# Kernel optimization log

Measured on AMD Instinct MI355X. Metric: run time of the kernel, lower is better.

## Reference

```python
import jax, jax.numpy as jnp
import numpy as np

N, C, H, W = 64, 64, 128, 128
KH, KW = 3, 3


def setup_inputs() -> dict:
    key = jax.random.key(0)
    k1, k2 = jax.random.split(key)
    images = jax.random.normal(k1, (N, C, H, W), dtype=jnp.float32)
    kernels = jax.random.normal(k2, (N, C, KH, KW), dtype=jnp.float32)
    return {"images": images, "kernels": kernels}


def reference(images, kernels):
    # Per-sample conv: image i ([C,H,W]) convolved with kernel i ([C,kh,kw]) -> 1 channel.
    # Equivalent to a grouped conv with N groups:
    #   input  [1, N*C, H, W], weights [N, C, kh, kw], feature_group_count=N
    n, c, h, w = images.shape
    x = images.reshape(1, n * c, h, w)
    out = jax.lax.conv_general_dilated(
        x, kernels,
        window_strides=(1, 1),
        padding='VALID',
        dimension_numbers=('NCHW', 'OIHW', 'NCHW'),
        feature_group_count=n,
    )  # [1, N, H', W']
    return out.reshape(n, 1, out.shape[2], out.shape[3])
```

## Files before the change

kernel.cpp:

```cpp
#include <hip/hip_runtime.h>


#define NS   64
#define CCH  64
#define HH   128
#define WW   128
#define OHH  126
#define OWW  126
#define CHS  (HH * WW)

__global__ __launch_bounds__(256, 2)
void ImageWiseConv2d_direct(const float* __restrict__ img,
                            const float* __restrict__ ker,
                            float* __restrict__ out)
{
    const int tid = threadIdx.x;
    const int bx  = blockIdx.x;
    const int bt  = bx & 7;
    const int n   = bx >> 3;
    const int h0  = bt * 16;

    const int r0 = (tid >> 5) << 1;
    const int c0 = (tid & 31) << 2;

    int ihr = h0 + r0;
    if (ihr > HH - 4) ihr = HH - 4;
    const int bOff = (c0 < 124) ? 4 : 2;

    const float* p0 = img + (((n * CCH) * HH) + ihr) * WW + c0;
    const float* kp = ker + (n * CCH) * 9;

    float a00 = 0.f, a01 = 0.f, a02 = 0.f, a03 = 0.f;
    float a10 = 0.f, a11 = 0.f, a12 = 0.f, a13 = 0.f;

    float4 A0, A1, A2, A3;
    float2 B0, B1, B2, B3;
    A0 = *(const float4*)(p0);
    A1 = *(const float4*)(p0 + WW);
    A2 = *(const float4*)(p0 + 2 * WW);
    A3 = *(const float4*)(p0 + 3 * WW);
    B0 = *(const float2*)(p0 + bOff);
    B1 = *(const float2*)(p0 + WW + bOff);
    B2 = *(const float2*)(p0 + 2 * WW + bOff);
    B3 = *(const float2*)(p0 + 3 * WW + bOff);

    for (int c = 0; c < CCH; ++c) {
        float4 nA0, nA1, nA2, nA3;
        float2 nB0, nB1, nB2, nB3;
        const bool more = (c + 1 < CCH);
        if (more) {
            const float* q = p0 + (c + 1) * CHS;
            nA0 = *(const float4*)(q);
            nA1 = *(const float4*)(q + WW);
            nA2 = *(const float4*)(q + 2 * WW);
            nA3 = *(const float4*)(q + 3 * WW);
            nB0 = *(const float2*)(q + bOff);
            nB1 = *(const float2*)(q + WW + bOff);
            nB2 = *(const float2*)(q + 2 * WW + bOff);
            nB3 = *(const float2*)(q + 3 * WW + bOff);
        }

        const float w0 = kp[c * 9 + 0], w1 = kp[c * 9 + 1], w2 = kp[c * 9 + 2];
        const float w3 = kp[c * 9 + 3], w4 = kp[c * 9 + 4], w5 = kp[c * 9 + 5];
        const float w6 = kp[c * 9 + 6], w7 = kp[c * 9 + 7], w8 = kp[c * 9 + 8];

        {
            const float v0 = A0.x, v1 = A0.y, v2 = A0.z, v3 = A0.w, v4 = B0.x, v5 = B0.y;
            a00 = fmaf(w0, v0, a00); a00 = fmaf(w1, v1, a00); a00 = fmaf(w2, v2, a00);
            a01 = fmaf(w0, v1, a01); a01 = fmaf(w1, v2, a01); a01 = fmaf(w2, v3, a01);
            a02 = fmaf(w0, v2, a02); a02 = fmaf(w1, v3, a02); a02 = fmaf(w2, v4, a02);
            a03 = fmaf(w0, v3, a03); a03 = fmaf(w1, v4, a03); a03 = fmaf(w2, v5, a03);
        }
        {
            const float v0 = A1.x, v1 = A1.y, v2 = A1.z, v3 = A1.w, v4 = B1.x, v5 = B1.y;
            a00 = fmaf(w3, v0, a00); a00 = fmaf(w4, v1, a00); a00 = fmaf(w5, v2, a00);
            a01 = fmaf(w3, v1, a01); a01 = fmaf(w4, v2, a01); a01 = fmaf(w5, v3, a01);
            a02 = fmaf(w3, v2, a02); a02 = fmaf(w4, v3, a02); a02 = fmaf(w5, v4, a02);
            a03 = fmaf(w3, v3, a03); a03 = fmaf(w4, v4, a03); a03 = fmaf(w5, v5, a03);
            a10 = fmaf(w0, v0, a10); a10 = fmaf(w1, v1, a10); a10 = fmaf(w2, v2, a10);
            a11 = fmaf(w0, v1, a11); a11 = fmaf(w1, v2, a11); a11 = fmaf(w2, v3, a11);
            a12 = fmaf(w0, v2, a12); a12 = fmaf(w1, v3, a12); a12 = fmaf(w2, v4, a12);
            a13 = fmaf(w0, v3, a13); a13 = fmaf(w1, v4, a13); a13 = fmaf(w2, v5, a13);
        }
        {
            const float v0 = A2.x, v1 = A2.y, v2 = A2.z, v3 = A2.w, v4 = B2.x, v5 = B2.y;
            a00 = fmaf(w6, v0, a00); a00 = fmaf(w7, v1, a00); a00 = fmaf(w8, v2, a00);
            a01 = fmaf(w6, v1, a01); a01 = fmaf(w7, v2, a01); a01 = fmaf(w8, v3, a01);
            a02 = fmaf(w6, v2, a02); a02 = fmaf(w7, v3, a02); a02 = fmaf(w8, v4, a02);
            a03 = fmaf(w6, v3, a03); a03 = fmaf(w7, v4, a03); a03 = fmaf(w8, v5, a03);
            a10 = fmaf(w3, v0, a10); a10 = fmaf(w4, v1, a10); a10 = fmaf(w5, v2, a10);
            a11 = fmaf(w3, v1, a11); a11 = fmaf(w4, v2, a11); a11 = fmaf(w5, v3, a11);
            a12 = fmaf(w3, v2, a12); a12 = fmaf(w4, v3, a12); a12 = fmaf(w5, v4, a12);
            a13 = fmaf(w3, v3, a13); a13 = fmaf(w4, v4, a13); a13 = fmaf(w5, v5, a13);
        }
        {
            const float v0 = A3.x, v1 = A3.y, v2 = A3.z, v3 = A3.w, v4 = B3.x, v5 = B3.y;
            a10 = fmaf(w6, v0, a10); a10 = fmaf(w7, v1, a10); a10 = fmaf(w8, v2, a10);
            a11 = fmaf(w6, v1, a11); a11 = fmaf(w7, v2, a11); a11 = fmaf(w8, v3, a11);
            a12 = fmaf(w6, v2, a12); a12 = fmaf(w7, v3, a12); a12 = fmaf(w8, v4, a12);
            a13 = fmaf(w6, v3, a13); a13 = fmaf(w7, v4, a13); a13 = fmaf(w8, v5, a13);
        }

        if (more) {
            A0 = nA0; A1 = nA1; A2 = nA2; A3 = nA3;
            B0 = nB0; B1 = nB1; B2 = nB2; B3 = nB3;
        }
    }

    const int oh0 = h0 + r0;
    if (oh0 < OHH) {
        float* o0 = out + (n * OHH + oh0) * OWW + c0;
        float* o1 = o0 + OWW;
        *(float2*)o0 = make_float2(a00, a01);
        *(float2*)o1 = make_float2(a10, a11);
        if (c0 < 124) {
            *(float2*)(o0 + 2) = make_float2(a02, a03);
            *(float2*)(o1 + 2) = make_float2(a12, a13);
        }
    }
}

extern "C" void kernel_launch(void* const* d_in, const int* in_sizes, int n_in,
                              void* d_out, int out_size, void* d_ws, size_t ws_size,
                              hipStream_t stream) {
    const float* img = (const float*)d_in[0];
    const float* ker = (const float*)d_in[1];
    float* out = (float*)d_out;

    ImageWiseConv2d_direct<<<dim3(NS * 8), dim3(256), 0, stream>>>(img, ker, out);
}
```

Baseline: 356.7 us.

## Split channel reduction across four groups with partial buffers and a reduce kernel

The input channels are split into four groups of 16, so the main kernel launches four times as many blocks, each writing a partial sum into a padded workspace. A second kernel adds the four partials into the output. The aim is to raise occupancy and memory-level parallelism for what looks like a bandwidth-bound kernel that was underfilling the GPU with 512 blocks. The cost is extra partial-buffer traffic, a second kernel launch, and a dependence on the workspace being large enough.

Result: no change. 363.6 us (+1.9%).

```diff
diff --git a/kernel.cpp b/kernel.cpp
--- a/kernel.cpp
+++ b/kernel.cpp
@@ -8,16 +8,20 @@
 #define OHH  126
 #define OWW  126
 #define CHS  (HH * WW)
+#define NG   4
+#define CPG  16
+#define PSTR 128
 
 __global__ __launch_bounds__(256, 2)
-void ImageWiseConv2d_direct(const float* __restrict__ img,
-                            const float* __restrict__ ker,
-                            float* __restrict__ out)
+void ImageWiseConv2d_main(const float* __restrict__ img,
+                          const float* __restrict__ ker,
+                          float* __restrict__ part)
 {
     const int tid = threadIdx.x;
     const int bx  = blockIdx.x;
     const int bt  = bx & 7;
-    const int n   = bx >> 3;
+    const int n   = (bx >> 3) & 63;
+    const int g   = bx >> 9;
     const int h0  = bt * 16;
 
     const int r0 = (tid >> 5) << 1;
@@ -27,8 +31,9 @@
     if (ihr > HH - 4) ihr = HH - 4;
     const int bOff = (c0 < 124) ? 4 : 2;
 
-    const float* p0 = img + (((n * CCH) * HH) + ihr) * WW + c0;
-    const float* kp = ker + (n * CCH) * 9;
+    const int cb = n * CCH + g * CPG;
+    const float* p0 = img + ((cb * HH) + ihr) * WW + c0;
+    const float* kp = ker + cb * 9;
 
     float a00 = 0.f, a01 = 0.f, a02 = 0.f, a03 = 0.f;
     float a10 = 0.f, a11 = 0.f, a12 = 0.f, a13 = 0.f;
@@ -44,10 +49,10 @@
     B2 = *(const float2*)(p0 + 2 * WW + bOff);
     B3 = *(const float2*)(p0 + 3 * WW + bOff);
 
-    for (int c = 0; c < CCH; ++c) {
+    for (int c = 0; c < CPG; ++c) {
         float4 nA0, nA1, nA2, nA3;
         float2 nB0, nB1, nB2, nB3;
-        const bool more = (c + 1 < CCH);
+        const bool more = (c + 1 < CPG);
         if (more) {
             const float* q = p0 + (c + 1) * CHS;
             nA0 = *(const float4*)(q);
@@ -109,15 +114,29 @@
 
     const int oh0 = h0 + r0;
     if (oh0 < OHH) {
-        float* o0 = out + (n * OHH + oh0) * OWW + c0;
-        float* o1 = o0 + OWW;
-        *(float2*)o0 = make_float2(a00, a01);
-        *(float2*)o1 = make_float2(a10, a11);
-        if (c0 < 124) {
-            *(float2*)(o0 + 2) = make_float2(a02, a03);
-            *(float2*)(o1 + 2) = make_float2(a12, a13);
-        }
+        float* pp = part + (((g * NS + n) * OHH) + oh0) * PSTR + c0;
+        *(float4*)pp = make_float4(a00, a01, a02, a03);
     }
+    if (oh0 + 1 < OHH) {
+        float* pp = part + (((g * NS + n) * OHH) + oh0 + 1) * PSTR + c0;
+        *(float4*)pp = make_float4(a10, a11, a12, a13);
+    }
+}
+
+__global__ __launch_bounds__(256)
+void ImageWiseConv2d_reduce(const float* __restrict__ part,
+                            float* __restrict__ out)
+{
+    const int i = blockIdx.x * 256 + threadIdx.x;
+    const int total = NS * OHH * OWW;
+    if (i >= total) return;
+    const int n  = i / (OHH * OWW);
+    const int r  = i - n * (OHH * OWW);
+    const int oh = r / OWW;
+    const int ow = r - oh * OWW;
+    const int gs = NS * OHH * PSTR;
+    const int pb = (n * OHH + oh) * PSTR + ow;
+    out[i] = (part[pb] + part[pb + gs]) + (part[pb + 2 * gs] + part[pb + 3 * gs]);
 }
 
 extern "C" void kernel_launch(void* const* d_in, const int* in_sizes, int n_in,
@@ -125,7 +144,11 @@
                               hipStream_t stream) {
     const float* img = (const float*)d_in[0];
     const float* ker = (const float*)d_in[1];
-    float* out = (float*)d_out;
+    float* out  = (float*)d_out;
+    float* part = (float*)d_ws;
 
-    ImageWiseConv2d_direct<<<dim3(NS * 8), dim3(256), 0, stream>>>(img, ker, out);
+    ImageWiseConv2d_main<<<dim3(NG * NS * 8), dim3(256), 0, stream>>>(img, ker, part);
+
+    const int total = NS * OHH * OWW;
+    ImageWiseConv2d_reduce<<<dim3((total + 255) / 256), dim3(256), 0, stream>>>(part, out);
 }
```
